# Optimization experiments

Hardware: AMD Instinct MI355X
Metric: run time of the kernel (lower is better)

Reference implementation:

```python
import jax, jax.numpy as jnp
import numpy as np

T, B, E, H = 2048, 2, 2048, 16
HD = E // H
SCALE = HD ** -0.5
NEG = -1e9  # large-negative additive mask (finite, safe in fp32/bf16)


def setup_inputs() -> dict:
    key = jax.random.key(0)
    ks = jax.random.split(key, 6)
    query = jax.random.normal(ks[0], (T, B, E), dtype=jnp.float32)
    # causal additive mask, as metaseq builds for decoder self-attention
    attn_mask = jnp.where(jnp.tril(jnp.ones((T, T), dtype=bool)), 0.0, NEG).astype(jnp.float32)
    # combined qkv projection: rows ordered [K | V | Q] per split_tensor_along_last_dim
    qkv_w = jax.random.normal(ks[1], (3 * E, E), dtype=jnp.float32) * (1.0 / np.sqrt(2 * E))
    qkv_b = jax.random.uniform(ks[2], (3 * E,), dtype=jnp.float32, minval=-1, maxval=1) / np.sqrt(E)
    out_w = jax.random.normal(ks[3], (E, E), dtype=jnp.float32) * (1.0 / np.sqrt(2 * E))
    out_b = jax.random.uniform(ks[4], (E,), dtype=jnp.float32, minval=-1, maxval=1) / np.sqrt(E)
    return {"query": query, "attn_mask": attn_mask, "qkv_w": qkv_w,
            "qkv_b": qkv_b, "out_w": out_w, "out_b": out_b}


def reference(query, attn_mask, qkv_w, qkv_b, out_w, out_b):
    t, b, e = query.shape
    # fused QKV projection (ColumnParallelLinear, world_size=1)
    kvq = jnp.einsum('tbe,fe->tbf', query, qkv_w) + qkv_b  # [T,B,3E]
    k, v, q = kvq[..., :e], kvq[..., e:2 * e], kvq[..., 2 * e:]
    q = q * SCALE
    q = q.reshape(t, b, H, HD)
    k = k.reshape(t, b, H, HD)
    v = v.reshape(t, b, H, HD)
    # explicit QK^T bmm -> [B,H,T,S]
    scores = jnp.einsum('tbhd,sbhd->bhts', q, k) + attn_mask[None, None]
    probs = jax.nn.softmax(scores, axis=-1)  # dropout p=0 -> identity
    ctx = jnp.einsum('bhts,sbhd->tbhd', probs, v).reshape(t, b, e)
    # RowParallelLinear out_proj (skip_bias_add in the original; bias added here)
    out = jnp.einsum('tbe,fe->tbf', ctx, out_w) + out_b
    return out
```

## Files before the change

kernel.cpp:

```cpp
#include <hip/hip_runtime.h>
#include <hip/hip_bf16.h>
#include <stdint.h>

#define T_DIM 2048
#define B_DIM 2
#define E_DIM 2048
#define H_DIM 16
#define HD_DIM 128
#define F_DIM 6144
#define F2   4096
#define ROWS 4096
#define KVB 64

#define QK_SCALE 0.08838834764831845f
#define LOG2E    1.4426950408889634f
#define RESCALE_THR 8.0f

typedef __bf16 bf16_t;
typedef __bf16 bf16x8 __attribute__((ext_vector_type(8)));
typedef __bf16 bf16x4 __attribute__((ext_vector_type(4)));
typedef float  f32x4  __attribute__((ext_vector_type(4)));

__device__ __forceinline__ void gll16(const void* g, void* l) {
  __builtin_amdgcn_global_load_lds((const __attribute__((address_space(1))) void*)g,
                                   (__attribute__((address_space(3))) void*)l, 16, 0, 0);
}

__global__ void cvt3(const float* __restrict__ s0, bf16_t* __restrict__ d0, int n0,
                     const float* __restrict__ s1, bf16_t* __restrict__ d1, int n1,
                     const float* __restrict__ s2, bf16_t* __restrict__ d2, int n2) {
  int total = n0 + n1 + n2;
  int i = blockIdx.x * blockDim.x + threadIdx.x;
  int stride = gridDim.x * blockDim.x;
  for (; i < total; i += stride) {
    const float* s; bf16_t* d; int j;
    if (i < n0)            { s = s0; d = d0; j = i; }
    else if (i < n0 + n1)  { s = s1; d = d1; j = i - n0; }
    else                   { s = s2; d = d2; j = i - n0 - n1; }
    float4 v = ((const float4*)s)[j];
    bf16x4 o;
    o[0] = (bf16_t)v.x; o[1] = (bf16_t)v.y; o[2] = (bf16_t)v.z; o[3] = (bf16_t)v.w;
    ((bf16x4*)d)[j] = o;
  }
}

__launch_bounds__(256, 2)
__global__ void gemm_qkv(const bf16_t* __restrict__ A, const bf16_t* __restrict__ Bm,
                         const float* __restrict__ bias, bf16_t* __restrict__ KVQ2,
                         bf16_t* __restrict__ VTg)
{
  __shared__ __align__(16) bf16_t Sm[2][128][64];
  bf16_t* Tp = &Sm[0][0][0];
  const int K = E_DIM, nbn = 48;

  int bid = blockIdx.x;
  int cpx = gridDim.x >> 3;
  int swz = (bid & 7) * cpx + (bid >> 3);
  int bm = swz / nbn, bn = swz % nbn;

  int tid = threadIdx.x;
  int lane = tid & 63, wid = tid >> 6;
  int lr = lane & 15, lg = lane >> 4;
  int wm = wid >> 1, wn = wid & 1;

  f32x4 acc[4][4] = {};

  int srow8 = tid >> 3;
  int schunk = tid & 7;

  const bf16_t* gA = A + (size_t)(bm * 128) * K;
  const bf16_t* gB = Bm + (size_t)(bn * 128) * K;

  for (int k0 = 0; k0 < K; k0 += 64) {
    #pragma unroll
    for (int i = 0; i < 4; ++i) {
      int row = i * 32 + srow8;
      int sc = schunk ^ (row & 7);
      gll16(gA + (size_t)row * K + k0 + sc * 8, &Sm[0][row][schunk * 8]);
    }
    #pragma unroll
    for (int i = 0; i < 4; ++i) {
      int row = i * 32 + srow8;
      int sc = schunk ^ (row & 7);
      gll16(gB + (size_t)row * K + k0 + sc * 8, &Sm[1][row][schunk * 8]);
    }
    __syncthreads();

    #pragma unroll
    for (int kk = 0; kk < 2; ++kk) {
      bf16x8 af[4], bfr[4];
      #pragma unroll
      for (int mi = 0; mi < 4; ++mi) {
        int row = wm * 64 + mi * 16 + lr;
        int ch = (kk * 4 + lg) ^ (row & 7);
        af[mi] = *(const bf16x8*)&Sm[0][row][ch * 8];
      }
      #pragma unroll
      for (int ni = 0; ni < 4; ++ni) {
        int row = wn * 64 + ni * 16 + lr;
        int ch = (kk * 4 + lg) ^ (row & 7);
        bfr[ni] = *(const bf16x8*)&Sm[1][row][ch * 8];
      }
      #pragma unroll
      for (int mi = 0; mi < 4; ++mi)
        #pragma unroll
        for (int ni = 0; ni < 4; ++ni)
          acc[mi][ni] = __builtin_amdgcn_mfma_f32_16x16x32_bf16(af[mi], bfr[ni], acc[mi][ni], 0, 0, 0);
    }
    __syncthreads();
  }

  if (bn >= 16 && bn < 32) {
    int h = bn - 16;
    #pragma unroll
    for (int mi = 0; mi < 4; ++mi) {
      int row0 = wm * 64 + mi * 16 + lg * 4;
      #pragma unroll
      for (int ni = 0; ni < 4; ++ni) {
        int lc = wn * 64 + ni * 16 + lr;
        float bv = bias[bn * 128 + lc];
        bf16x4 pk;
        #pragma unroll
        for (int r = 0; r < 4; ++r) pk[r] = (bf16_t)(acc[mi][ni][r] + bv);
        int rowX = row0 ^ ((lc & 15) << 3);
        *(bf16x4*)&Tp[lc * 128 + rowX] = pk;
      }
    }
    __syncthreads();
    int d = tid >> 1, half = tid & 1;
    int sz = (d & 15) << 3;
    size_t tb = (size_t)bm * 64 + half * 32;
    bf16_t* o0 = VTg + ((size_t)h        * 128 + d) * T_DIM + tb;
    bf16_t* o1 = VTg + ((size_t)(16 + h) * 128 + d) * T_DIM + tb;
    #pragma unroll
    for (int kk = 0; kk < 4; ++kk) {
      int rl = half * 64 + kk * 16;
      bf16x8 v0 = *(const bf16x8*)&Tp[d * 128 + ((rl)     ^ sz)];
      bf16x8 v1 = *(const bf16x8*)&Tp[d * 128 + ((rl + 8) ^ sz)];
      bf16x8 ev, od;
      #pragma unroll
      for (int j = 0; j < 4; ++j) {
        ev[j] = v0[2 * j];     ev[4 + j] = v1[2 * j];
        od[j] = v0[2 * j + 1]; od[4 + j] = v1[2 * j + 1];
      }
      *(bf16x8*)(o0 + kk * 8) = ev;
      *(bf16x8*)(o1 + kk * 8) = od;
    }
  } else {
    bool isQ = (bn >= 32);
    float scl = isQ ? (QK_SCALE * LOG2E) : 1.0f;
    int colOff = isQ ? -2048 : 0;
    #pragma unroll
    for (int mi = 0; mi < 4; ++mi) {
      int row0 = bm * 128 + wm * 64 + mi * 16 + lg * 4;
      #pragma unroll
      for (int ni = 0; ni < 4; ++ni) {
        int col = bn * 128 + wn * 64 + ni * 16 + lr;
        float bv = bias[col];
        #pragma unroll
        for (int r = 0; r < 4; ++r) {
          float v = (acc[mi][ni][r] + bv) * scl;
          KVQ2[(size_t)(row0 + r) * F2 + col + colOff] = (bf16_t)v;
        }
      }
    }
  }
}

__launch_bounds__(256, 2)
__global__ void gemm_out(const bf16_t* __restrict__ A, const bf16_t* __restrict__ Bm,
                         const float* __restrict__ bias, float* __restrict__ Cout)
{
  __shared__ __align__(16) bf16_t As[128][64];
  __shared__ __align__(16) bf16_t Bs[128][64];
  const int K = E_DIM, N = E_DIM, nbn = 16;

  int bid = blockIdx.x;
  int cpx = gridDim.x >> 3;
  int swz = (bid & 7) * cpx + (bid >> 3);
  int bm = swz / nbn, bn = swz % nbn;

  int tid = threadIdx.x;
  int lane = tid & 63, wid = tid >> 6;
  int lr = lane & 15, lg = lane >> 4;
  int wm = wid >> 1, wn = wid & 1;

  f32x4 acc[4][4] = {};
  int srow8 = tid >> 3, schunk = tid & 7;

  const bf16_t* gA = A + (size_t)(bm * 128) * K;
  const bf16_t* gB = Bm + (size_t)(bn * 128) * K;

  for (int k0 = 0; k0 < K; k0 += 64) {
    #pragma unroll
    for (int i = 0; i < 4; ++i) {
      int row = i * 32 + srow8;
      int sc = schunk ^ (row & 7);
      gll16(gA + (size_t)row * K + k0 + sc * 8, &As[row][schunk * 8]);
    }
    #pragma unroll
    for (int i = 0; i < 4; ++i) {
      int row = i * 32 + srow8;
      int sc = schunk ^ (row & 7);
      gll16(gB + (size_t)row * K + k0 + sc * 8, &Bs[row][schunk * 8]);
    }
    __syncthreads();

    #pragma unroll
    for (int kk = 0; kk < 2; ++kk) {
      bf16x8 af[4], bfr[4];
      #pragma unroll
      for (int mi = 0; mi < 4; ++mi) {
        int row = wm * 64 + mi * 16 + lr;
        int ch = (kk * 4 + lg) ^ (row & 7);
        af[mi] = *(const bf16x8*)&As[row][ch * 8];
      }
      #pragma unroll
      for (int ni = 0; ni < 4; ++ni) {
        int row = wn * 64 + ni * 16 + lr;
        int ch = (kk * 4 + lg) ^ (row & 7);
        bfr[ni] = *(const bf16x8*)&Bs[row][ch * 8];
      }
      #pragma unroll
      for (int mi = 0; mi < 4; ++mi)
        #pragma unroll
        for (int ni = 0; ni < 4; ++ni)
          acc[mi][ni] = __builtin_amdgcn_mfma_f32_16x16x32_bf16(af[mi], bfr[ni], acc[mi][ni], 0, 0, 0);
    }
    __syncthreads();
  }

  #pragma unroll
  for (int mi = 0; mi < 4; ++mi) {
    int row0 = bm * 128 + wm * 64 + mi * 16 + lg * 4;
    #pragma unroll
    for (int ni = 0; ni < 4; ++ni) {
      int col = bn * 128 + wn * 64 + ni * 16 + lr;
      float bv = bias[col];
      #pragma unroll
      for (int r = 0; r < 4; ++r)
        Cout[(size_t)(row0 + r) * N + col] = acc[mi][ni][r] + bv;
    }
  }
}

__launch_bounds__(256, 2)
__global__ void attn4(const bf16_t* __restrict__ KVQ2, const bf16_t* __restrict__ VTg,
                      bf16_t* __restrict__ CTX)
{
  __shared__ __align__(16) bf16_t Ks[2][KVB][128];
  __shared__ __align__(16) bf16_t Vs[2][128][KVB];
  __shared__ __align__(16) bf16_t Ps[4][2][16][64];

  int bid = blockIdx.x;
  int xcd = bid & 7;
  int j   = bid >> 3;
  int hi  = j >> 5;
  int mid = (j >> 4) & 1;
  int q   = j & 15;
  int bh  = xcd * 4 + hi * 2 + mid;
  int qt  = hi ? (15 - q) : q;
  int b = bh >> 4, h = bh & 15;

  int tid = threadIdx.x;
  int lane = tid & 63, wid = tid >> 6;
  int lr = lane & 15, lg = lane >> 4;

  const bf16_t* kbase = KVQ2 + (size_t)b * F2 + (size_t)h * HD_DIM;
  const bf16_t* vtb   = VTg + (size_t)bh * HD_DIM * T_DIM;

  bf16x8 qf[2][4];
  #pragma unroll
  for (int mf = 0; mf < 2; ++mf) {
    int t = qt * 128 + wid * 32 + mf * 16 + lr;
    const bf16_t* qb = KVQ2 + ((size_t)t * B_DIM + b) * F2 + E_DIM + h * HD_DIM;
    #pragma unroll
    for (int ks = 0; ks < 4; ++ks) qf[mf][ks] = *(const bf16x8*)(qb + ks * 32 + lg * 8);
  }

  f32x4 ctxa[2][8] = {};
  float mR[2] = { -1e30f, -1e30f };
  float lR[2] = { 0.0f, 0.0f };

  int krow = tid >> 4, kch = tid & 15;
  int vrow = tid >> 3, vch = tid & 7;

  auto stage = [&](int buf, int it) {
    int s0 = it * KVB;
    #pragma unroll
    for (int i = 0; i < 4; ++i) {
      int row = i * 16 + krow;
      int sc = kch ^ (row & 7);
      gll16(kbase + (size_t)(s0 + row) * B_DIM * F2 + sc * 8, &Ks[buf][row][kch * 8]);
    }
    #pragma unroll
    for (int i = 0; i < 4; ++i) {
      int row = i * 32 + vrow;
      int sc = vch ^ (row & 7);
      gll16(vtb + (size_t)row * T_DIM + s0 + sc * 8, &Vs[buf][row][vch * 8]);
    }
  };

  int nt = 2 * (qt + 1);
  stage(0, 0);
  __syncthreads();

  int tqw = qt * 128 + wid * 32;

  for (int it = 0; it < nt; ++it) {
    int cur = it & 1;
    if (it + 1 < nt) stage(cur ^ 1, it + 1);
    int s0 = it * KVB;
    bool diag = (it >= nt - 2);

    f32x4 sacc[2][4] = {};
    __builtin_amdgcn_s_setprio(1);
    #pragma unroll
    for (int ks = 0; ks < 4; ++ks) {
      #pragma unroll
      for (int nti = 0; nti < 4; ++nti) {
        int srow = nti * 16 + lr;
        int slot = (ks * 4 + lg) ^ (srow & 7);
        bf16x8 kf = *(const bf16x8*)&Ks[cur][srow][slot * 8];
        sacc[0][nti] = __builtin_amdgcn_mfma_f32_16x16x32_bf16(kf, qf[0][ks], sacc[0][nti], 0, 0, 0);
        sacc[1][nti] = __builtin_amdgcn_mfma_f32_16x16x32_bf16(kf, qf[1][ks], sacc[1][nti], 0, 0, 0);
      }
    }
    __builtin_amdgcn_s_setprio(0);

    float mxl = -1e30f;
    #pragma unroll
    for (int mf = 0; mf < 2; ++mf) {
      int qg = tqw + mf * 16 + lr;
      #pragma unroll
      for (int nti = 0; nti < 4; ++nti)
        #pragma unroll
        for (int r = 0; r < 4; ++r) {
          float v = sacc[mf][nti][r];
          if (diag) v = (s0 + nti * 16 + lg * 4 + r > qg) ? -1e30f : v;
          sacc[mf][nti][r] = v;
          mxl = fmaxf(mxl, v - mR[mf]);
        }
    }
    if (!__all(mxl <= RESCALE_THR)) {
      #pragma unroll
      for (int mf = 0; mf < 2; ++mf) {
        float mx = -1e30f;
        #pragma unroll
        for (int nti = 0; nti < 4; ++nti)
          #pragma unroll
          for (int r = 0; r < 4; ++r) mx = fmaxf(mx, sacc[mf][nti][r]);
        mx = fmaxf(mx, __shfl_xor(mx, 16, 64));
        mx = fmaxf(mx, __shfl_xor(mx, 32, 64));
        float mn = fmaxf(mR[mf], mx);
        float rs = exp2f(mR[mf] - mn);
        mR[mf] = mn;
        lR[mf] *= rs;
        #pragma unroll
        for (int dt = 0; dt < 8; ++dt) ctxa[mf][dt] *= rs;
      }
    }
    #pragma unroll
    for (int mf = 0; mf < 2; ++mf)
      #pragma unroll
      for (int nti = 0; nti < 4; ++nti) {
        bf16x4 pk;
        float ps = 0.0f;
        #pragma unroll
        for (int r = 0; r < 4; ++r) {
          float p = exp2f(sacc[mf][nti][r] - mR[mf]);
          ps += p;
          pk[r] = (bf16_t)p;
        }
        lR[mf] += ps;
        int cS = (nti * 2 + (lg >> 1)) ^ (lr & 7);
        *(bf16x4*)&Ps[wid][mf][lr][cS * 8 + (lg & 1) * 4] = pk;
      }
    asm volatile("s_waitcnt lgkmcnt(0)" ::: "memory");
    __builtin_amdgcn_sched_barrier(0);

    bf16x8 pb[2][2];
    #pragma unroll
    for (int mf = 0; mf < 2; ++mf)
      #pragma unroll
      for (int kh = 0; kh < 2; ++kh)
        pb[mf][kh] = *(const bf16x8*)&Ps[wid][mf][lr][(((kh * 4 + lg)) ^ (lr & 7)) * 8];
    __builtin_amdgcn_s_setprio(1);
    #pragma unroll
    for (int dt = 0; dt < 8; ++dt) {
      int drow = dt * 16 + lr;
      int sl0 = lg ^ (drow & 7);
      int sl1 = (4 + lg) ^ (drow & 7);
      bf16x8 vf0 = *(const bf16x8*)&Vs[cur][drow][sl0 * 8];
      bf16x8 vf1 = *(const bf16x8*)&Vs[cur][drow][sl1 * 8];
      ctxa[0][dt] = __builtin_amdgcn_mfma_f32_16x16x32_bf16(vf0, pb[0][0], ctxa[0][dt], 0, 0, 0);
      ctxa[0][dt] = __builtin_amdgcn_mfma_f32_16x16x32_bf16(vf1, pb[0][1], ctxa[0][dt], 0, 0, 0);
      ctxa[1][dt] = __builtin_amdgcn_mfma_f32_16x16x32_bf16(vf0, pb[1][0], ctxa[1][dt], 0, 0, 0);
      ctxa[1][dt] = __builtin_amdgcn_mfma_f32_16x16x32_bf16(vf1, pb[1][1], ctxa[1][dt], 0, 0, 0);
    }
    __builtin_amdgcn_s_setprio(0);

    __syncthreads();
  }

  #pragma unroll
  for (int mf = 0; mf < 2; ++mf) {
    lR[mf] += __shfl_xor(lR[mf], 16, 64);
    lR[mf] += __shfl_xor(lR[mf], 32, 64);
    float inv = 1.0f / lR[mf];
    int t = tqw + mf * 16 + lr;
    bf16_t* out = CTX + ((size_t)t * B_DIM + b) * E_DIM + h * HD_DIM;
    #pragma unroll
    for (int dt = 0; dt < 8; ++dt) {
      bf16x4 pk;
      #pragma unroll
      for (int r = 0; r < 4; ++r) pk[r] = (bf16_t)(ctxa[mf][dt][r] * inv);
      *(bf16x4*)(out + dt * 16 + lg * 4) = pk;
    }
  }
}

extern "C" void kernel_launch(void* const* d_in, const int* in_sizes, int n_in,
                              void* d_out, int out_size, void* d_ws, size_t ws_size,
                              hipStream_t stream)
{
  const float* query = (const float*)d_in[0];
  const float* qkv_w = (const float*)d_in[2];
  const float* qkv_b = (const float*)d_in[3];
  const float* out_w = (const float*)d_in[4];
  const float* out_b = (const float*)d_in[5];

  bf16_t* Xbf  = (bf16_t*)d_ws;
  bf16_t* Wqkv = Xbf  + (size_t)ROWS * E_DIM;
  bf16_t* Wout = Wqkv + (size_t)F_DIM * E_DIM;
  bf16_t* KVQ2 = Wout + (size_t)E_DIM * E_DIM;
  bf16_t* VTg  = KVQ2 + (size_t)ROWS * F2;
  bf16_t* CTX  = Xbf;

  cvt3<<<2048, 256, 0, stream>>>(query, Xbf,  ROWS * E_DIM / 4,
                                 qkv_w, Wqkv, F_DIM * E_DIM / 4,
                                 out_w, Wout, E_DIM * E_DIM / 4);

  gemm_qkv<<<32 * 48, 256, 0, stream>>>(Xbf, Wqkv, qkv_b, KVQ2, VTg);

  attn4<<<512, 256, 0, stream>>>(KVQ2, VTg, CTX);

  gemm_out<<<32 * 16, 256, 0, stream>>>(CTX, Wout, out_b, (float*)d_out);
}
```

Measured before the change: 265.7 us.

## Enlarge attention query tile to 256 rows per block with half-split KV processing

The attention kernel now gives each block 256 query rows, 64 per wave, instead of 128, halving the grid to 256 blocks. Each 64-key tile is processed in two 32-key halves so register pressure stays manageable, and each K/V fragment read from LDS feeds four MFMAs instead of two. The aim is to cut redundant K/V loads and LDS traffic per unit of work. In exchange, occupancy drops to one block per CU, causal load balance gets worse because the heavy/light tile pairing was removed, and only 256 blocks run on a 256-CU part.

```diff
diff --git a/kernel.cpp b/kernel.cpp
--- a/kernel.cpp
+++ b/kernel.cpp
@@ -244,22 +244,19 @@
   }
 }
 
-__launch_bounds__(256, 2)
-__global__ void attn4(const bf16_t* __restrict__ KVQ2, const bf16_t* __restrict__ VTg,
+__launch_bounds__(256, 1)
+__global__ void attn5(const bf16_t* __restrict__ KVQ2, const bf16_t* __restrict__ VTg,
                       bf16_t* __restrict__ CTX)
 {
   __shared__ __align__(16) bf16_t Ks[2][KVB][128];
   __shared__ __align__(16) bf16_t Vs[2][128][KVB];
-  __shared__ __align__(16) bf16_t Ps[4][2][16][64];
+  __shared__ __align__(16) bf16_t Ps[4][4][16][64];
 
   int bid = blockIdx.x;
   int xcd = bid & 7;
   int j   = bid >> 3;
-  int hi  = j >> 5;
-  int mid = (j >> 4) & 1;
-  int q   = j & 15;
-  int bh  = xcd * 4 + hi * 2 + mid;
-  int qt  = hi ? (15 - q) : q;
+  int bh  = xcd * 4 + (j >> 3);
+  int qt  = j & 7;
   int b = bh >> 4, h = bh & 15;
 
   int tid = threadIdx.x;
@@ -269,18 +266,18 @@
   const bf16_t* kbase = KVQ2 + (size_t)b * F2 + (size_t)h * HD_DIM;
   const bf16_t* vtb   = VTg + (size_t)bh * HD_DIM * T_DIM;
 
-  bf16x8 qf[2][4];
+  bf16x8 qf[4][4];
   #pragma unroll
-  for (int mf = 0; mf < 2; ++mf) {
-    int t = qt * 128 + wid * 32 + mf * 16 + lr;
+  for (int mf = 0; mf < 4; ++mf) {
+    int t = qt * 256 + wid * 64 + mf * 16 + lr;
     const bf16_t* qb = KVQ2 + ((size_t)t * B_DIM + b) * F2 + E_DIM + h * HD_DIM;
     #pragma unroll
     for (int ks = 0; ks < 4; ++ks) qf[mf][ks] = *(const bf16x8*)(qb + ks * 32 + lg * 8);
   }
 
-  f32x4 ctxa[2][8] = {};
-  float mR[2] = { -1e30f, -1e30f };
-  float lR[2] = { 0.0f, 0.0f };
+  f32x4 ctxa[4][8] = {};
+  float mR[4] = { -1e30f, -1e30f, -1e30f, -1e30f };
+  float lR[4] = {};
 
   int krow = tid >> 4, kch = tid & 15;
   int vrow = tid >> 3, vch = tid & 7;
@@ -301,110 +298,111 @@
     }
   };
 
-  int nt = 2 * (qt + 1);
+  int nt = 4 * (qt + 1);
   stage(0, 0);
   __syncthreads();
 
-  int tqw = qt * 128 + wid * 32;
+  int tqw = qt * 256 + wid * 64;
 
   for (int it = 0; it < nt; ++it) {
     int cur = it & 1;
     if (it + 1 < nt) stage(cur ^ 1, it + 1);
-    int s0 = it * KVB;
-    bool diag = (it >= nt - 2);
-
-    f32x4 sacc[2][4] = {};
-    __builtin_amdgcn_s_setprio(1);
-    #pragma unroll
-    for (int ks = 0; ks < 4; ++ks) {
-      #pragma unroll
-      for (int nti = 0; nti < 4; ++nti) {
-        int srow = nti * 16 + lr;
-        int slot = (ks * 4 + lg) ^ (srow & 7);
-        bf16x8 kf = *(const bf16x8*)&Ks[cur][srow][slot * 8];
-        sacc[0][nti] = __builtin_amdgcn_mfma_f32_16x16x32_bf16(kf, qf[0][ks], sacc[0][nti], 0, 0, 0);
-        sacc[1][nti] = __builtin_amdgcn_mfma_f32_16x16x32_bf16(kf, qf[1][ks], sacc[1][nti], 0, 0, 0);
-      }
-    }
-    __builtin_amdgcn_s_setprio(0);
-
-    float mxl = -1e30f;
-    #pragma unroll
-    for (int mf = 0; mf < 2; ++mf) {
-      int qg = tqw + mf * 16 + lr;
-      #pragma unroll
-      for (int nti = 0; nti < 4; ++nti)
-        #pragma unroll
-        for (int r = 0; r < 4; ++r) {
-          float v = sacc[mf][nti][r];
-          if (diag) v = (s0 + nti * 16 + lg * 4 + r > qg) ? -1e30f : v;
-          sacc[mf][nti][r] = v;
-          mxl = fmaxf(mxl, v - mR[mf]);
+    bool diag = (it >= nt - 4);
+
+    #pragma unroll
+    for (int sh = 0; sh < 2; ++sh) {
+      int s0s = it * KVB + sh * 32;
+
+      f32x4 sacc[4][2] = {};
+      __builtin_amdgcn_s_setprio(1);
+      #pragma unroll
+      for (int ks = 0; ks < 4; ++ks) {
+        #pragma unroll
+        for (int ntl = 0; ntl < 2; ++ntl) {
+          int srow = sh * 32 + ntl * 16 + lr;
+          int slot = (ks * 4 + lg) ^ (srow & 7);
+          bf16x8 kf = *(const bf16x8*)&Ks[cur][srow][slot * 8];
+          #pragma unroll
+          for (int mf = 0; mf < 4; ++mf)
+            sacc[mf][ntl] = __builtin_amdgcn_mfma_f32_16x16x32_bf16(kf, qf[mf][ks], sacc[mf][ntl], 0, 0, 0);
         }
-    }
-    if (!__all(mxl <= RESCALE_THR)) {
-      #pragma unroll
-      for (int mf = 0; mf < 2; ++mf) {
-        float mx = -1e30f;
-        #pragma unroll
-        for (int nti = 0; nti < 4; ++nti)
+      }
+      __builtin_amdgcn_s_setprio(0);
+
+      float mxl = -1e30f;
+      #pragma unroll
+      for (int mf = 0; mf < 4; ++mf) {
+        int qg = tqw + mf * 16 + lr;
+        #pragma unroll
+        for (int ntl = 0; ntl < 2; ++ntl)
           #pragma unroll
-          for (int r = 0; r < 4; ++r) mx = fmaxf(mx, sacc[mf][nti][r]);
-        mx = fmaxf(mx, __shfl_xor(mx, 16, 64));
-        mx = fmaxf(mx, __shfl_xor(mx, 32, 64));
-        float mn = fmaxf(mR[mf], mx);
-        float rs = exp2f(mR[mf] - mn);
-        mR[mf] = mn;
-        lR[mf] *= rs;
-        #pragma unroll
-        for (int dt = 0; dt < 8; ++dt) ctxa[mf][dt] *= rs;
-      }
-    }
-    #pragma unroll
-    for (int mf = 0; mf < 2; ++mf)
-      #pragma unroll
-      for (int nti = 0; nti < 4; ++nti) {
-        bf16x4 pk;
-        float ps = 0.0f;
-        #pragma unroll
-        for (int r = 0; r < 4; ++r) {
-          float p = exp2f(sacc[mf][nti][r] - mR[mf]);
-          ps += p;
-          pk[r] = (bf16_t)p;
+          for (int r = 0; r < 4; ++r) {
+            float v = sacc[mf][ntl][r];
+            if (diag) v = (s0s + ntl * 16 + lg * 4 + r > qg) ? -1e30f : v;
+            sacc[mf][ntl][r] = v;
+            mxl = fmaxf(mxl, v - mR[mf]);
+          }
+      }
+      if (!__all(mxl <= RESCALE_THR)) {
+        #pragma unroll
+        for (int mf = 0; mf < 4; ++mf) {
+          float mx = -1e30f;
+          #pragma unroll
+          for (int ntl = 0; ntl < 2; ++ntl)
+            #pragma unroll
+            for (int r = 0; r < 4; ++r) mx = fmaxf(mx, sacc[mf][ntl][r]);
+          mx = fmaxf(mx, __shfl_xor(mx, 16, 64));
+          mx = fmaxf(mx, __shfl_xor(mx, 32, 64));
+          float mn = fmaxf(mR[mf], mx);
+          float rs = exp2f(mR[mf] - mn);
+          mR[mf] = mn;
+          lR[mf] *= rs;
+          #pragma unroll
+          for (int dt = 0; dt < 8; ++dt) ctxa[mf][dt] *= rs;
         }
-        lR[mf] += ps;
-        int cS = (nti * 2 + (lg >> 1)) ^ (lr & 7);
-        *(bf16x4*)&Ps[wid][mf][lr][cS * 8 + (lg & 1) * 4] = pk;
-      }
-    asm volatile("s_waitcnt lgkmcnt(0)" ::: "memory");
-    __builtin_amdgcn_sched_barrier(0);
-
-    bf16x8 pb[2][2];
-    #pragma unroll
-    for (int mf = 0; mf < 2; ++mf)
-      #pragma unroll
-      for (int kh = 0; kh < 2; ++kh)
-        pb[mf][kh] = *(const bf16x8*)&Ps[wid][mf][lr][(((kh * 4 + lg)) ^ (lr & 7)) * 8];
-    __builtin_amdgcn_s_setprio(1);
-    #pragma unroll
-    for (int dt = 0; dt < 8; ++dt) {
-      int drow = dt * 16 + lr;
-      int sl0 = lg ^ (drow & 7);
-      int sl1 = (4 + lg) ^ (drow & 7);
-      bf16x8 vf0 = *(const bf16x8*)&Vs[cur][drow][sl0 * 8];
-      bf16x8 vf1 = *(const bf16x8*)&Vs[cur][drow][sl1 * 8];
-      ctxa[0][dt] = __builtin_amdgcn_mfma_f32_16x16x32_bf16(vf0, pb[0][0], ctxa[0][dt], 0, 0, 0);
-      ctxa[0][dt] = __builtin_amdgcn_mfma_f32_16x16x32_bf16(vf1, pb[0][1], ctxa[0][dt], 0, 0, 0);
-      ctxa[1][dt] = __builtin_amdgcn_mfma_f32_16x16x32_bf16(vf0, pb[1][0], ctxa[1][dt], 0, 0, 0);
-      ctxa[1][dt] = __builtin_amdgcn_mfma_f32_16x16x32_bf16(vf1, pb[1][1], ctxa[1][dt], 0, 0, 0);
-    }
-    __builtin_amdgcn_s_setprio(0);
+      }
+      #pragma unroll
+      for (int mf = 0; mf < 4; ++mf)
+        #pragma unroll
+        for (int ntl = 0; ntl < 2; ++ntl) {
+          int nti = sh * 2 + ntl;
+          bf16x4 pk;
+          float ps = 0.0f;
+          #pragma unroll
+          for (int r = 0; r < 4; ++r) {
+            float p = exp2f(sacc[mf][ntl][r] - mR[mf]);
+            ps += p;
+            pk[r] = (bf16_t)p;
+          }
+          lR[mf] += ps;
+          int cS = (nti * 2 + (lg >> 1)) ^ (lr & 7);
+          *(bf16x4*)&Ps[wid][mf][lr][cS * 8 + (lg & 1) * 4] = pk;
+        }
+      asm volatile("s_waitcnt lgkmcnt(0)" ::: "memory");
+      __builtin_amdgcn_sched_barrier(0);
+
+      bf16x8 pb[4];
+      #pragma unroll
+      for (int mf = 0; mf < 4; ++mf)
+        pb[mf] = *(const bf16x8*)&Ps[wid][mf][lr][(((sh * 4 + lg)) ^ (lr & 7)) * 8];
+      __builtin_amdgcn_s_setprio(1);
+      #pragma unroll
+      for (int dt = 0; dt < 8; ++dt) {
+        int drow = dt * 16 + lr;
+        int sl = (sh * 4 + lg) ^ (drow & 7);
+        bf16x8 vf = *(const bf16x8*)&Vs[cur][drow][sl * 8];
+        #pragma unroll
+        for (int mf = 0; mf < 4; ++mf)
+          ctxa[mf][dt] = __builtin_amdgcn_mfma_f32_16x16x32_bf16(vf, pb[mf], ctxa[mf][dt], 0, 0, 0);
+      }
+      __builtin_amdgcn_s_setprio(0);
+    }
 
     __syncthreads();
   }
 
   #pragma unroll
-  for (int mf = 0; mf < 2; ++mf) {
+  for (int mf = 0; mf < 4; ++mf) {
     lR[mf] += __shfl_xor(lR[mf], 16, 64);
     lR[mf] += __shfl_xor(lR[mf], 32, 64);
     float inv = 1.0f / lR[mf];
@@ -443,7 +441,7 @@
 
   gemm_qkv<<<32 * 48, 256, 0, stream>>>(Xbf, Wqkv, qkv_b, KVQ2, VTg);
 
-  attn4<<<512, 256, 0, stream>>>(KVQ2, VTg, CTX);
+  attn5<<<256, 256, 0, stream>>>(KVQ2, VTg, CTX);
 
   gemm_out<<<32 * 16, 256, 0, stream>>>(CTX, Wout, out_b, (float*)d_out);
 }
```

After: 323.6 us. 21.8% more time.

## Triple-buffer attention K/V tiles with half-size blocks and explicit vmcnt waits

Applied to the files above, without the earlier changes.

Shrinks the attention KV tile from 64 to 32 keys and moves from double to triple buffering in LDS. Loads are issued two iterations ahead, and each iteration ends with a partial vmcnt wait plus a raw s_barrier instead of a full __syncthreads. The aim is to hide global-to-LDS latency better, at the cost of twice as many loop iterations, more per-iteration softmax and barrier overhead, and smaller MFMA batches per step.

```diff
diff --git a/kernel.cpp b/kernel.cpp
--- a/kernel.cpp
+++ b/kernel.cpp
@@ -10,7 +10,7 @@
 #define F_DIM 6144
 #define F2   4096
 #define ROWS 4096
-#define KVB 64
+#define KVB 32
 
 #define QK_SCALE 0.08838834764831845f
 #define LOG2E    1.4426950408889634f
@@ -245,12 +245,12 @@
 }
 
 __launch_bounds__(256, 2)
-__global__ void attn4(const bf16_t* __restrict__ KVQ2, const bf16_t* __restrict__ VTg,
+__global__ void attn6(const bf16_t* __restrict__ KVQ2, const bf16_t* __restrict__ VTg,
                       bf16_t* __restrict__ CTX)
 {
-  __shared__ __align__(16) bf16_t Ks[2][KVB][128];
-  __shared__ __align__(16) bf16_t Vs[2][128][KVB];
-  __shared__ __align__(16) bf16_t Ps[4][2][16][64];
+  __shared__ __align__(16) bf16_t Ks[3][KVB][128];
+  __shared__ __align__(16) bf16_t Vs[3][128][KVB];
+  __shared__ __align__(16) bf16_t Ps[4][2][16][32];
 
   int bid = blockIdx.x;
   int xcd = bid & 7;
@@ -283,47 +283,50 @@
   float lR[2] = { 0.0f, 0.0f };
 
   int krow = tid >> 4, kch = tid & 15;
-  int vrow = tid >> 3, vch = tid & 7;
+  int vrow = tid >> 2, vch = tid & 3;
 
   auto stage = [&](int buf, int it) {
     int s0 = it * KVB;
     #pragma unroll
-    for (int i = 0; i < 4; ++i) {
+    for (int i = 0; i < 2; ++i) {
       int row = i * 16 + krow;
       int sc = kch ^ (row & 7);
       gll16(kbase + (size_t)(s0 + row) * B_DIM * F2 + sc * 8, &Ks[buf][row][kch * 8]);
     }
     #pragma unroll
-    for (int i = 0; i < 4; ++i) {
-      int row = i * 32 + vrow;
-      int sc = vch ^ (row & 7);
+    for (int i = 0; i < 2; ++i) {
+      int row = i * 64 + vrow;
+      int sc = vch ^ (row & 3);
       gll16(vtb + (size_t)row * T_DIM + s0 + sc * 8, &Vs[buf][row][vch * 8]);
     }
   };
 
-  int nt = 2 * (qt + 1);
+  int nt = 4 * (qt + 1);
   stage(0, 0);
-  __syncthreads();
+  stage(1, 1);
+  asm volatile("s_waitcnt vmcnt(4)" ::: "memory");
+  __builtin_amdgcn_sched_barrier(0);
+  __builtin_amdgcn_s_barrier();
 
   int tqw = qt * 128 + wid * 32;
 
   for (int it = 0; it < nt; ++it) {
-    int cur = it & 1;
-    if (it + 1 < nt) stage(cur ^ 1, it + 1);
+    int cur = it % 3;
+    if (it + 2 < nt) stage((it + 2) % 3, it + 2);
     int s0 = it * KVB;
-    bool diag = (it >= nt - 2);
-
-    f32x4 sacc[2][4] = {};
+    bool diag = (it >= nt - 4);
+
+    f32x4 sacc[2][2] = {};
     __builtin_amdgcn_s_setprio(1);
     #pragma unroll
     for (int ks = 0; ks < 4; ++ks) {
       #pragma unroll
-      for (int nti = 0; nti < 4; ++nti) {
-        int srow = nti * 16 + lr;
+      for (int ntl = 0; ntl < 2; ++ntl) {
+        int srow = ntl * 16 + lr;
         int slot = (ks * 4 + lg) ^ (srow & 7);
         bf16x8 kf = *(const bf16x8*)&Ks[cur][srow][slot * 8];
-        sacc[0][nti] = __builtin_amdgcn_mfma_f32_16x16x32_bf16(kf, qf[0][ks], sacc[0][nti], 0, 0, 0);
-        sacc[1][nti] = __builtin_amdgcn_mfma_f32_16x16x32_bf16(kf, qf[1][ks], sacc[1][nti], 0, 0, 0);
+        sacc[0][ntl] = __builtin_amdgcn_mfma_f32_16x16x32_bf16(kf, qf[0][ks], sacc[0][ntl], 0, 0, 0);
+        sacc[1][ntl] = __builtin_amdgcn_mfma_f32_16x16x32_bf16(kf, qf[1][ks], sacc[1][ntl], 0, 0, 0);
       }
     }
     __builtin_amdgcn_s_setprio(0);
@@ -333,12 +336,12 @@
     for (int mf = 0; mf < 2; ++mf) {
       int qg = tqw + mf * 16 + lr;
       #pragma unroll
-      for (int nti = 0; nti < 4; ++nti)
+      for (int ntl = 0; ntl < 2; ++ntl)
         #pragma unroll
         for (int r = 0; r < 4; ++r) {
-          float v = sacc[mf][nti][r];
-          if (diag) v = (s0 + nti * 16 + lg * 4 + r > qg) ? -1e30f : v;
-          sacc[mf][nti][r] = v;
+          float v = sacc[mf][ntl][r];
+          if (diag) v = (s0 + ntl * 16 + lg * 4 + r > qg) ? -1e30f : v;
+          sacc[mf][ntl][r] = v;
           mxl = fmaxf(mxl, v - mR[mf]);
         }
     }
@@ -347,9 +350,9 @@
       for (int mf = 0; mf < 2; ++mf) {
         float mx = -1e30f;
         #pragma unroll
-        for (int nti = 0; nti < 4; ++nti)
+        for (int ntl = 0; ntl < 2; ++ntl)
           #pragma unroll
-          for (int r = 0; r < 4; ++r) mx = fmaxf(mx, sacc[mf][nti][r]);
+          for (int r = 0; r < 4; ++r) mx = fmaxf(mx, sacc[mf][ntl][r]);
         mx = fmaxf(mx, __shfl_xor(mx, 16, 64));
         mx = fmaxf(mx, __shfl_xor(mx, 32, 64));
         float mn = fmaxf(mR[mf], mx);
@@ -363,44 +366,44 @@
     #pragma unroll
     for (int mf = 0; mf < 2; ++mf)
       #pragma unroll
-      for (int nti = 0; nti < 4; ++nti) {
+      for (int ntl = 0; ntl < 2; ++ntl) {
         bf16x4 pk;
         float ps = 0.0f;
         #pragma unroll
         for (int r = 0; r < 4; ++r) {
-          float p = exp2f(sacc[mf][nti][r] - mR[mf]);
+          float p = exp2f(sacc[mf][ntl][r] - mR[mf]);
           ps += p;
           pk[r] = (bf16_t)p;
         }
         lR[mf] += ps;
-        int cS = (nti * 2 + (lg >> 1)) ^ (lr & 7);
+        int cS = (ntl * 2 + (lg >> 1)) ^ (lr & 3);
         *(bf16x4*)&Ps[wid][mf][lr][cS * 8 + (lg & 1) * 4] = pk;
       }
     asm volatile("s_waitcnt lgkmcnt(0)" ::: "memory");
     __builtin_amdgcn_sched_barrier(0);
 
-    bf16x8 pb[2][2];
+    bf16x8 pb[2];
     #pragma unroll
     for (int mf = 0; mf < 2; ++mf)
-      #pragma unroll
-      for (int kh = 0; kh < 2; ++kh)
-        pb[mf][kh] = *(const bf16x8*)&Ps[wid][mf][lr][(((kh * 4 + lg)) ^ (lr & 7)) * 8];
+      pb[mf] = *(const bf16x8*)&Ps[wid][mf][lr][((lg) ^ (lr & 3)) * 8];
     __builtin_amdgcn_s_setprio(1);
     #pragma unroll
     for (int dt = 0; dt < 8; ++dt) {
       int drow = dt * 16 + lr;
-      int sl0 = lg ^ (drow & 7);
-      int sl1 = (4 + lg) ^ (drow & 7);
-      bf16x8 vf0 = *(const bf16x8*)&Vs[cur][drow][sl0 * 8];
-      bf16x8 vf1 = *(const bf16x8*)&Vs[cur][drow][sl1 * 8];
-      ctxa[0][dt] = __builtin_amdgcn_mfma_f32_16x16x32_bf16(vf0, pb[0][0], ctxa[0][dt], 0, 0, 0);
-      ctxa[0][dt] = __builtin_amdgcn_mfma_f32_16x16x32_bf16(vf1, pb[0][1], ctxa[0][dt], 0, 0, 0);
-      ctxa[1][dt] = __builtin_amdgcn_mfma_f32_16x16x32_bf16(vf0, pb[1][0], ctxa[1][dt], 0, 0, 0);
-      ctxa[1][dt] = __builtin_amdgcn_mfma_f32_16x16x32_bf16(vf1, pb[1][1], ctxa[1][dt], 0, 0, 0);
+      int sl = lg ^ (drow & 3);
+      bf16x8 vf = *(const bf16x8*)&Vs[cur][drow][sl * 8];
+      ctxa[0][dt] = __builtin_amdgcn_mfma_f32_16x16x32_bf16(vf, pb[0], ctxa[0][dt], 0, 0, 0);
+      ctxa[1][dt] = __builtin_amdgcn_mfma_f32_16x16x32_bf16(vf, pb[1], ctxa[1][dt], 0, 0, 0);
     }
     __builtin_amdgcn_s_setprio(0);
 
-    __syncthreads();
+    if (it + 2 < nt) {
+      asm volatile("s_waitcnt vmcnt(4)" ::: "memory");
+    } else if (it + 1 < nt) {
+      asm volatile("s_waitcnt vmcnt(0)" ::: "memory");
+    }
+    __builtin_amdgcn_sched_barrier(0);
+    __builtin_amdgcn_s_barrier();
   }
 
   #pragma unroll
@@ -443,7 +446,7 @@
 
   gemm_qkv<<<32 * 48, 256, 0, stream>>>(Xbf, Wqkv, qkv_b, KVQ2, VTg);
 
-  attn4<<<512, 256, 0, stream>>>(KVQ2, VTg, CTX);
+  attn6<<<512, 256, 0, stream>>>(KVQ2, VTg, CTX);
 
   gemm_out<<<32 * 16, 256, 0, stream>>>(CTX, Wout, out_b, (float*)d_out);
 }
```

Result: slower. 281.1 us (+5.8%).
